# Kernel tuning notes

Hardware: AMD Instinct MI355X
Metric: run time of the kernel (lower is better)

Reference implementation:

```python
import math
import jax, jax.numpy as jnp
import numpy as np

DN = ('NCHW', 'OIHW', 'NCHW')

def _conv2d(x, w, b, stride, padding='VALID'):
    y = jax.lax.conv_general_dilated(x, w, window_strides=stride, padding=padding,
                                     dimension_numbers=DN)
    return y + b[None, :, None, None]

def _same_padding_conv(x, w, b, s):
    # replicate torch same_padding_conv: ceil-mode SAME padding, then VALID conv
    H, W = x.shape[2], x.shape[3]
    kh, kw = w.shape[2], w.shape[3]
    out_h, out_w = math.ceil(H / s[0]), math.ceil(W / s[1])
    pad_h = max((out_h - 1) * s[0] + kh - H, 0)
    pad_w = max((out_w - 1) * s[1] + kw - W, 0)
    pt, pl = pad_h // 2, pad_w // 2
    x = jnp.pad(x, ((0, 0), (0, 0), (pt, pad_h - pt), (pl, pad_w - pl)))
    return _conv2d(x, w, b, s)

def _leaky(x):
    return jax.nn.leaky_relu(x, negative_slope=0.2)

def setup_inputs() -> dict:
    key = jax.random.key(0)
    ks = jax.random.split(key, 8)
    B, cin, cout, H, W = 2, 16, 24, 384, 1280
    fl = jax.random.normal(ks[0], (B, cin, H, W), jnp.float32)
    fr = jax.random.normal(ks[1], (B, cin, H, W), jnp.float32)
    w_em = jax.random.normal(ks[2], (cout, cin, 4, 4), jnp.float32) * 0.05
    b_em = jax.random.normal(ks[3], (cout,), jnp.float32) * 0.05
    w_rc = jax.random.normal(ks[4], (cout, cout, 1, 1), jnp.float32) * 0.1
    b_rc = jax.random.normal(ks[5], (cout,), jnp.float32) * 0.05
    w_tf = jax.random.normal(ks[6], (13, cout + 1, 1, 1), jnp.float32) * 0.1
    b_tf = jax.random.normal(ks[7], (13,), jnp.float32) * 0.05
    return {'feature_left': fl, 'feature_right': fr, 'max_disp': 64,
            'w_em': w_em, 'b_em': b_em, 'w_rc': w_rc, 'b_rc': b_rc,
            'w_tf': w_tf, 'b_tf': b_tf}

def reference(feature_left, feature_right, max_disp, w_em, b_em, w_rc, b_rc, w_tf, b_tf):
    # left branch: 4x4 conv, stride (4,4), VALID (torch default padding=0)
    fl = _leaky(_conv2d(_leaky(_conv2d(feature_left, w_em, b_em, (4, 4))), w_rc, b_rc, (1, 1)))
    # right branch: same-padding conv with stride (4,1) -> full width retained
    fr = _leaky(_conv2d(_leaky(_same_padding_conv(feature_right, w_em, b_em, (4, 1))), w_rc, b_rc, (1, 1)))
    B, C, Hq, Wq = fl.shape
    Wr = fr.shape[3]
    # clipped gather indices: idx[d, x] = clip(4*x - d + 1, 0, Wr-1)
    d = jnp.arange(max_disp)[:, None]          # [D,1]
    x = jnp.arange(Wq)[None, :]                # [1,Wq]
    idx = jnp.clip(4 * x - d + 1, 0, Wr - 1)   # [D,Wq]
    fr_g = jnp.take(fr, idx, axis=3)           # [B,C,H,D,Wq]
    # L1 cost over channels -> [B,D,H,Wq]
    cost_volume = jnp.sum(jnp.abs(fl[:, :, :, None, :] - fr_g), axis=1).transpose(0, 2, 1, 3)
    cost_f = jnp.min(cost_volume, axis=1, keepdims=True)                  # [B,1,H,Wq]
    d_init = jnp.argmin(cost_volume, axis=1, keepdims=True).astype(fl.dtype)
    p_init = jnp.concatenate([cost_f, fl], axis=1)
    p_init = _leaky(_conv2d(p_init, w_tf, b_tf, (1, 1)))                  # [B,13,H,Wq]
    z = jnp.zeros_like(d_init)
    out = jnp.concatenate([d_init, z, z, p_init], axis=1)                 # [B,16,H,Wq]
    return out, cost_volume
```

## Files before the change

kernel.cpp:

```cpp
#include <hip/hip_runtime.h>

#define B_   2
#define CIN  16
#define HIN  384
#define WIN  1280
#define CO   24
#define HQ   96
#define WL   320
#define WR   1280
#define DMAX 64

__device__ __forceinline__ float lk(float v) { return v >= 0.f ? v : 0.2f * v; }

__global__ __launch_bounds__(256) void k_left(
    const float* __restrict__ x, const float* __restrict__ w_em,
    const float* __restrict__ b_em, const float* __restrict__ w_rc,
    const float* __restrict__ b_rc, float* __restrict__ out)
{
    __shared__ float smem[CO * CIN * 16];
    __shared__ __align__(16) float swt[CO * CO];
    __shared__ float sbe[CO], sbr[CO];

    for (int i = threadIdx.x; i < CO * CIN * 16; i += 256) smem[i] = w_em[i];
    for (int i = threadIdx.x; i < CO * CO; i += 256) swt[i] = w_rc[(i % CO) * CO + (i / CO)];
    if (threadIdx.x < CO) { sbe[threadIdx.x] = b_em[threadIdx.x]; sbr[threadIdx.x] = b_rc[threadIdx.x]; }
    __syncthreads();

    const int t = threadIdx.x;
    const int half = t >> 7, pxl = t & 127;
    const int obase = half * 12;
    const int flat = blockIdx.x * 128 + pxl;
    const int j = flat % WL, h = (flat / WL) % HQ, b = flat / (WL * HQ);

    float acc[12];
#pragma unroll
    for (int oo = 0; oo < 12; ++oo) acc[oo] = sbe[obase + oo];

    for (int c = 0; c < CIN; ++c) {
#pragma unroll
        for (int kh = 0; kh < 4; ++kh) {
            const float4 v = *(const float4*)(x + ((size_t)(b * CIN + c) * HIN + 4 * h + kh) * WIN + 4 * j);
#pragma unroll
            for (int oo = 0; oo < 12; ++oo) {
                const float4 wv = *(const float4*)&smem[(((obase + oo) * CIN + c) * 4 + kh) * 4];
                float a = acc[oo];
                a = fmaf(v.x, wv.x, a);
                a = fmaf(v.y, wv.y, a);
                a = fmaf(v.z, wv.z, a);
                a = fmaf(v.w, wv.w, a);
                acc[oo] = a;
            }
        }
    }
    __syncthreads();
#pragma unroll
    for (int oo = 0; oo < 12; ++oo) smem[(obase + oo) * 128 + pxl] = lk(acc[oo]);
    __syncthreads();

    float acc2[12];
#pragma unroll
    for (int oo = 0; oo < 12; ++oo) acc2[oo] = sbr[obase + oo];
    for (int c = 0; c < CO; ++c) {
        const float in_c = smem[c * 128 + pxl];
#pragma unroll
        for (int m = 0; m < 3; ++m) {
            const float4 wv = *(const float4*)&swt[c * CO + obase + 4 * m];
            acc2[4 * m + 0] = fmaf(in_c, wv.x, acc2[4 * m + 0]);
            acc2[4 * m + 1] = fmaf(in_c, wv.y, acc2[4 * m + 1]);
            acc2[4 * m + 2] = fmaf(in_c, wv.z, acc2[4 * m + 2]);
            acc2[4 * m + 3] = fmaf(in_c, wv.w, acc2[4 * m + 3]);
        }
    }
#pragma unroll
    for (int oo = 0; oo < 12; ++oo)
        out[((size_t)(b * CO + obase + oo) * HQ + h) * WL + j] = lk(acc2[oo]);
}

__global__ __launch_bounds__(256) void k_right(
    const float* __restrict__ x, const float* __restrict__ w_em,
    const float* __restrict__ b_em, const float* __restrict__ w_rc,
    const float* __restrict__ b_rc, float* __restrict__ out)
{
    __shared__ __align__(16) float sw[CO * CIN * 16];
    __shared__ __align__(16) float swt[CO * CO];
    __shared__ float sbe[CO], sbr[CO];

    for (int i = threadIdx.x; i < CO * CIN * 16; i += 256) sw[i] = w_em[i];
    for (int i = threadIdx.x; i < CO * CO; i += 256) swt[i] = w_rc[(i % CO) * CO + (i / CO)];
    if (threadIdx.x < CO) { sbe[threadIdx.x] = b_em[threadIdx.x]; sbr[threadIdx.x] = b_rc[threadIdx.x]; }
    __syncthreads();

    const int t = threadIdx.x;
    const int L = t & 63, quarter = t >> 6;
    const int obase = quarter * 6;
    const int row = blockIdx.x / 5, jbase = (blockIdx.x % 5) * 256;
    const int b = row / HQ, h = row % HQ;

    const bool vm1 = (jbase + 4 * L) > 0;
    const bool vp  = (jbase + 4 * L + 4) < WIN;
    const int  om1 = vm1 ? (4 * L - 2) : 0;
    const int  op4 = vp  ? (4 * L + 4) : 0;

    float acc[4][6];
#pragma unroll
    for (int k = 0; k < 4; ++k)
#pragma unroll
        for (int oo = 0; oo < 6; ++oo) acc[k][oo] = sbe[obase + oo];

    for (int c = 0; c < CIN; ++c) {
#pragma unroll
        for (int kh = 0; kh < 4; ++kh) {
            const float* xr = x + ((size_t)(b * CIN + c) * HIN + 4 * h + kh) * WIN + jbase;
            const float4  v = *(const float4*)(xr + 4 * L);
            const float2  A = *(const float2*)(xr + om1);
            const float2  C = *(const float2*)(xr + op4);
            float in[7];
            in[0] = vm1 ? A.y : 0.f;
            in[1] = v.x; in[2] = v.y; in[3] = v.z; in[4] = v.w;
            in[5] = vp ? C.x : 0.f;
            in[6] = vp ? C.y : 0.f;
#pragma unroll
            for (int oo = 0; oo < 6; ++oo) {
                const float4 wv = *(const float4*)&sw[(((obase + oo) * CIN + c) * 4 + kh) * 4];
#pragma unroll
                for (int k = 0; k < 4; ++k) {
                    float a = acc[k][oo];
                    a = fmaf(in[k],     wv.x, a);
                    a = fmaf(in[k + 1], wv.y, a);
                    a = fmaf(in[k + 2], wv.z, a);
                    a = fmaf(in[k + 3], wv.w, a);
                    acc[k][oo] = a;
                }
            }
        }
    }
    __syncthreads();
#pragma unroll
    for (int oo = 0; oo < 6; ++oo) {
        float4 st = make_float4(lk(acc[0][oo]), lk(acc[1][oo]), lk(acc[2][oo]), lk(acc[3][oo]));
        *(float4*)&sw[(obase + oo) * 256 + 4 * L] = st;
    }
    __syncthreads();

    float acc2[CO];
#pragma unroll
    for (int o = 0; o < CO; ++o) acc2[o] = sbr[o];
    for (int c = 0; c < CO; ++c) {
        const float in_c = sw[c * 256 + t];
#pragma unroll
        for (int m = 0; m < 6; ++m) {
            const float4 wv = *(const float4*)&swt[c * CO + 4 * m];
            acc2[4 * m + 0] = fmaf(in_c, wv.x, acc2[4 * m + 0]);
            acc2[4 * m + 1] = fmaf(in_c, wv.y, acc2[4 * m + 1]);
            acc2[4 * m + 2] = fmaf(in_c, wv.z, acc2[4 * m + 2]);
            acc2[4 * m + 3] = fmaf(in_c, wv.w, acc2[4 * m + 3]);
        }
    }
#pragma unroll
    for (int o = 0; o < CO; ++o)
        out[((size_t)(b * CO + o) * HQ + h) * WR + jbase + t] = lk(acc2[o]);
}

__global__ __launch_bounds__(256) void k_cost(
    const float* __restrict__ fl, const float* __restrict__ fr,
    const float* __restrict__ wtf, const float* __restrict__ btf,
    float* __restrict__ out, float* __restrict__ cost)
{
    __shared__ float frs[CO * 324];
    __shared__ float sbest[256];
    __shared__ int   sbd[256];

    const int t  = threadIdx.x;
    const int j  = t & 63;
    const int w  = t >> 6;
    const int jc = blockIdx.x % 5;
    const int r  = blockIdx.x / 5;
    const int h  = r % HQ, b = r / HQ;
    const int j0 = jc * 64;
    const int jg = j0 + j;
    const int colbase = 4 * j0 - 64;

    for (int idx = t; idx < CO * 320; idx += 256) {
        const int c = idx / 320, Wd = idx % 320;
        const int col = colbase + Wd;
        frs[c * 324 + 2 + Wd] = fr[((size_t)(b * CO + c) * HQ + h) * WR + (col > 0 ? col : 0)];
    }
    __syncthreads();

    float acc[4][4];
#pragma unroll
    for (int q = 0; q < 4; ++q)
#pragma unroll
        for (int rr = 0; rr < 4; ++rr) acc[q][rr] = 0.f;

    for (int c = 0; c < CO; ++c) {
        const float flc = fl[((size_t)(b * CO + c) * HQ + h) * WL + jg];
        const float* base = &frs[c * 324 + 4 * j + 64];
#pragma unroll
        for (int q = 0; q < 4; ++q) {
            const int D = 4 * w + q;
            const float4 v = *(const float4*)(base - 4 * D);
            acc[q][0] += fabsf(flc - v.w);
            acc[q][1] += fabsf(flc - v.z);
            acc[q][2] += fabsf(flc - v.y);
            acc[q][3] += fabsf(flc - v.x);
        }
    }

#pragma unroll
    for (int q = 0; q < 4; ++q)
#pragma unroll
        for (int rr = 0; rr < 4; ++rr) {
            const int d = 16 * w + 4 * q + rr;
            cost[((size_t)(b * DMAX + d) * HQ + h) * WL + jg] = acc[q][rr];
        }

    float best = acc[0][0]; int bd = 16 * w;
#pragma unroll
    for (int q = 0; q < 4; ++q)
#pragma unroll
        for (int rr = 0; rr < 4; ++rr) {
            if (q == 0 && rr == 0) continue;
            const int d = 16 * w + 4 * q + rr;
            if (acc[q][rr] < best) { best = acc[q][rr]; bd = d; }
        }
    sbest[t] = best; sbd[t] = bd;
    __syncthreads();

    if (t < 64) {
        float cur = sbest[j]; int curd = sbd[j];
#pragma unroll
        for (int g = 1; g < 4; ++g) {
            const float v = sbest[g * 64 + j];
            if (v < cur) { cur = v; curd = sbd[g * 64 + j]; }
        }
        float flr[CO];
#pragma unroll
        for (int c = 0; c < CO; ++c) flr[c] = fl[((size_t)(b * CO + c) * HQ + h) * WL + jg];
#pragma unroll
        for (int o = 0; o < 13; ++o) {
            float a = btf[o] + wtf[o * 25] * cur;
#pragma unroll
            for (int c = 0; c < CO; ++c) a += wtf[o * 25 + 1 + c] * flr[c];
            out[((size_t)(b * 16 + 3 + o) * HQ + h) * WL + jg] = lk(a);
        }
        out[((size_t)(b * 16 + 0) * HQ + h) * WL + jg] = (float)curd;
        out[((size_t)(b * 16 + 1) * HQ + h) * WL + jg] = 0.f;
        out[((size_t)(b * 16 + 2) * HQ + h) * WL + jg] = 0.f;
    }
}

extern "C" void kernel_launch(void* const* d_in, const int* in_sizes, int n_in,
                              void* d_out, int out_size, void* d_ws, size_t ws_size,
                              hipStream_t stream) {
    const float* fl_in = (const float*)d_in[0];
    const float* fr_in = (const float*)d_in[1];
    const float* w_em = (const float*)d_in[3];
    const float* b_em = (const float*)d_in[4];
    const float* w_rc = (const float*)d_in[5];
    const float* b_rc = (const float*)d_in[6];
    const float* w_tf = (const float*)d_in[7];
    const float* b_tf = (const float*)d_in[8];

    float* out  = (float*)d_out;
    float* cost = out + (size_t)B_ * 16 * HQ * WL;

    float* fl_ws = (float*)d_ws;
    float* fr_ws = fl_ws + (size_t)B_ * CO * HQ * WL;

    hipLaunchKernelGGL(k_right, dim3(960), dim3(256), 0, stream,
                       fr_in, w_em, b_em, w_rc, b_rc, fr_ws);
    hipLaunchKernelGGL(k_left,  dim3(480), dim3(256), 0, stream,
                       fl_in, w_em, b_em, w_rc, b_rc, fl_ws);
    hipLaunchKernelGGL(k_cost,  dim3(960), dim3(256), 0, stream,
                       fl_ws, fr_ws, w_tf, b_tf, out, cost);
}
```

Measured before the change: 252.1 us.

## Retile cost kernel for two-pixel register reuse and spread tail conv over warps

The cost-volume kernel now gives each thread two adjacent output columns and eight disparities. This lets it reuse overlapping right-feature float4 loads from shared memory and issue vectorized float2 loads and stores. The final 13-output 1x1 conv is split across all four wavefronts instead of one, which removes a serial tail. The left kernel's fma chains are also rewritten as plain multiply-add expressions, and the float4 weight reads in the second conv become scalar reads. The argmin now reduces over 8 groups, and changed float summation order in the left kernel may alter rounding slightly.

```diff
diff --git a/kernel.cpp b/kernel.cpp
--- a/kernel.cpp
+++ b/kernel.cpp
@@ -18,7 +18,7 @@
     const float* __restrict__ b_rc, float* __restrict__ out)
 {
     __shared__ float smem[CO * CIN * 16];
-    __shared__ __align__(16) float swt[CO * CO];
+    __shared__ float swt[CO * CO];
     __shared__ float sbe[CO], sbr[CO];
 
     for (int i = threadIdx.x; i < CO * CIN * 16; i += 256) smem[i] = w_em[i];
@@ -43,12 +43,7 @@
 #pragma unroll
             for (int oo = 0; oo < 12; ++oo) {
                 const float4 wv = *(const float4*)&smem[(((obase + oo) * CIN + c) * 4 + kh) * 4];
-                float a = acc[oo];
-                a = fmaf(v.x, wv.x, a);
-                a = fmaf(v.y, wv.y, a);
-                a = fmaf(v.z, wv.z, a);
-                a = fmaf(v.w, wv.w, a);
-                acc[oo] = a;
+                acc[oo] += v.x * wv.x + v.y * wv.y + v.z * wv.z + v.w * wv.w;
             }
         }
     }
@@ -63,13 +58,7 @@
     for (int c = 0; c < CO; ++c) {
         const float in_c = smem[c * 128 + pxl];
 #pragma unroll
-        for (int m = 0; m < 3; ++m) {
-            const float4 wv = *(const float4*)&swt[c * CO + obase + 4 * m];
-            acc2[4 * m + 0] = fmaf(in_c, wv.x, acc2[4 * m + 0]);
-            acc2[4 * m + 1] = fmaf(in_c, wv.y, acc2[4 * m + 1]);
-            acc2[4 * m + 2] = fmaf(in_c, wv.z, acc2[4 * m + 2]);
-            acc2[4 * m + 3] = fmaf(in_c, wv.w, acc2[4 * m + 3]);
-        }
+        for (int oo = 0; oo < 12; ++oo) acc2[oo] += in_c * swt[c * CO + obase + oo];
     }
 #pragma unroll
     for (int oo = 0; oo < 12; ++oo)
@@ -167,18 +156,18 @@
     float* __restrict__ out, float* __restrict__ cost)
 {
     __shared__ float frs[CO * 324];
-    __shared__ float sbest[256];
-    __shared__ int   sbd[256];
+    __shared__ float sbest[8 * 64];
+    __shared__ int   sbd[8 * 64];
 
     const int t  = threadIdx.x;
-    const int j  = t & 63;
-    const int w  = t >> 6;
+    const int p  = t & 31;
+    const int g  = t >> 5;
     const int jc = blockIdx.x % 5;
     const int r  = blockIdx.x / 5;
     const int h  = r % HQ, b = r / HQ;
     const int j0 = jc * 64;
-    const int jg = j0 + j;
     const int colbase = 4 * j0 - 64;
+    const int cA = 2 * p;
 
     for (int idx = t; idx < CO * 320; idx += 256) {
         const int c = idx / 320, Wd = idx % 320;
@@ -187,63 +176,73 @@
     }
     __syncthreads();
 
-    float acc[4][4];
-#pragma unroll
-    for (int q = 0; q < 4; ++q)
-#pragma unroll
-        for (int rr = 0; rr < 4; ++rr) acc[q][rr] = 0.f;
+    float accA[8], accB[8];
+#pragma unroll
+    for (int dd = 0; dd < 8; ++dd) { accA[dd] = 0.f; accB[dd] = 0.f; }
 
     for (int c = 0; c < CO; ++c) {
-        const float flc = fl[((size_t)(b * CO + c) * HQ + h) * WL + jg];
-        const float* base = &frs[c * 324 + 4 * j + 64];
-#pragma unroll
-        for (int q = 0; q < 4; ++q) {
-            const int D = 4 * w + q;
-            const float4 v = *(const float4*)(base - 4 * D);
-            acc[q][0] += fabsf(flc - v.w);
-            acc[q][1] += fabsf(flc - v.z);
-            acc[q][2] += fabsf(flc - v.y);
-            acc[q][3] += fabsf(flc - v.x);
-        }
-    }
-
-#pragma unroll
-    for (int q = 0; q < 4; ++q)
-#pragma unroll
-        for (int rr = 0; rr < 4; ++rr) {
-            const int d = 16 * w + 4 * q + rr;
-            cost[((size_t)(b * DMAX + d) * HQ + h) * WL + jg] = acc[q][rr];
-        }
-
-    float best = acc[0][0]; int bd = 16 * w;
-#pragma unroll
-    for (int q = 0; q < 4; ++q)
-#pragma unroll
-        for (int rr = 0; rr < 4; ++rr) {
-            if (q == 0 && rr == 0) continue;
-            const int d = 16 * w + 4 * q + rr;
-            if (acc[q][rr] < best) { best = acc[q][rr]; bd = d; }
-        }
-    sbest[t] = best; sbd[t] = bd;
-    __syncthreads();
-
-    if (t < 64) {
-        float cur = sbest[j]; int curd = sbd[j];
-#pragma unroll
-        for (int g = 1; g < 4; ++g) {
-            const float v = sbest[g * 64 + j];
-            if (v < cur) { cur = v; curd = sbd[g * 64 + j]; }
-        }
-        float flr[CO];
-#pragma unroll
-        for (int c = 0; c < CO; ++c) flr[c] = fl[((size_t)(b * CO + c) * HQ + h) * WL + jg];
-#pragma unroll
-        for (int o = 0; o < 13; ++o) {
-            float a = btf[o] + wtf[o * 25] * cur;
-#pragma unroll
-            for (int c = 0; c < CO; ++c) a += wtf[o * 25 + 1 + c] * flr[c];
-            out[((size_t)(b * 16 + 3 + o) * HQ + h) * WL + jg] = lk(a);
-        }
+        const float2 flc = *(const float2*)&fl[((size_t)(b * CO + c) * HQ + h) * WL + j0 + cA];
+        const float* base = &frs[c * 324 + 8 * p - 8 * g + 60];
+        const float4 F0 = *(const float4*)(base);
+        const float4 F1 = *(const float4*)(base + 4);
+        const float4 F2 = *(const float4*)(base + 8);
+        accA[0] += fabsf(flc.x - F1.w);
+        accA[1] += fabsf(flc.x - F1.z);
+        accA[2] += fabsf(flc.x - F1.y);
+        accA[3] += fabsf(flc.x - F1.x);
+        accA[4] += fabsf(flc.x - F0.w);
+        accA[5] += fabsf(flc.x - F0.z);
+        accA[6] += fabsf(flc.x - F0.y);
+        accA[7] += fabsf(flc.x - F0.x);
+        accB[0] += fabsf(flc.y - F2.w);
+        accB[1] += fabsf(flc.y - F2.z);
+        accB[2] += fabsf(flc.y - F2.y);
+        accB[3] += fabsf(flc.y - F2.x);
+        accB[4] += fabsf(flc.y - F1.w);
+        accB[5] += fabsf(flc.y - F1.z);
+        accB[6] += fabsf(flc.y - F1.y);
+        accB[7] += fabsf(flc.y - F1.x);
+    }
+
+#pragma unroll
+    for (int dd = 0; dd < 8; ++dd) {
+        const int d = 8 * g + dd;
+        float2 st = make_float2(accA[dd], accB[dd]);
+        *(float2*)&cost[((size_t)(b * DMAX + d) * HQ + h) * WL + j0 + cA] = st;
+    }
+
+    float bA = accA[0]; int dA = 8 * g;
+    float bB = accB[0]; int dB = 8 * g;
+#pragma unroll
+    for (int dd = 1; dd < 8; ++dd) {
+        if (accA[dd] < bA) { bA = accA[dd]; dA = 8 * g + dd; }
+        if (accB[dd] < bB) { bB = accB[dd]; dB = 8 * g + dd; }
+    }
+    sbest[g * 64 + cA]     = bA; sbd[g * 64 + cA]     = dA;
+    sbest[g * 64 + cA + 1] = bB; sbd[g * 64 + cA + 1] = dB;
+    __syncthreads();
+
+    const int j = t & 63, w = t >> 6;
+    const int jg = j0 + j;
+    float cur = sbest[j]; int curd = sbd[j];
+#pragma unroll
+    for (int g2 = 1; g2 < 8; ++g2) {
+        const float v = sbest[g2 * 64 + j];
+        if (v < cur) { cur = v; curd = sbd[g2 * 64 + j]; }
+    }
+    float flr[CO];
+#pragma unroll
+    for (int c = 0; c < CO; ++c) flr[c] = fl[((size_t)(b * CO + c) * HQ + h) * WL + jg];
+
+    const int o_lo = (w == 0) ? 0 : 4 * w - 3;
+    const int o_hi = 4 * w + 1;
+    for (int o = o_lo; o < o_hi; ++o) {
+        float a = btf[o] + wtf[o * 25] * cur;
+#pragma unroll
+        for (int c = 0; c < CO; ++c) a += wtf[o * 25 + 1 + c] * flr[c];
+        out[((size_t)(b * 16 + 3 + o) * HQ + h) * WL + jg] = lk(a);
+    }
+    if (w == 0) {
         out[((size_t)(b * 16 + 0) * HQ + h) * WL + jg] = (float)curd;
         out[((size_t)(b * 16 + 1) * HQ + h) * WL + jg] = 0.f;
         out[((size_t)(b * 16 + 2) * HQ + h) * WL + jg] = 0.f;
```

New measurement: 237.7 us. 5.7% less time.

## Merge left and right embedding kernels into one interleaved launch; spread 1x1 head across warps

Applied to the files above, without the earlier changes.

The separate left and right embedding kernels become one kernel of 1440 blocks. Every third block does a left tile and the rest do right tiles, so both branches run at once and one launch is removed. In the cost kernel, the final 13-output 1x1 conv is now split across all four wavefronts instead of only the first 64 threads. This cuts the serial tail, though every wavefront now reloads the 24 fl channels. The left path also swaps explicit fmaf chains for plain expressions, and mixing two block types in one kernel may raise register pressure.

```diff
diff --git a/kernel.cpp b/kernel.cpp
--- a/kernel.cpp
+++ b/kernel.cpp
@@ -12,153 +12,132 @@
 
 __device__ __forceinline__ float lk(float v) { return v >= 0.f ? v : 0.2f * v; }
 
-__global__ __launch_bounds__(256) void k_left(
-    const float* __restrict__ x, const float* __restrict__ w_em,
-    const float* __restrict__ b_em, const float* __restrict__ w_rc,
-    const float* __restrict__ b_rc, float* __restrict__ out)
+__global__ __launch_bounds__(256) void k_em(
+    const float* __restrict__ xl, const float* __restrict__ xr,
+    const float* __restrict__ w_em, const float* __restrict__ b_em,
+    const float* __restrict__ w_rc, const float* __restrict__ b_rc,
+    float* __restrict__ out_l, float* __restrict__ out_r)
 {
-    __shared__ float smem[CO * CIN * 16];
+    __shared__ __align__(16) float buf[CO * CIN * 16];
     __shared__ __align__(16) float swt[CO * CO];
     __shared__ float sbe[CO], sbr[CO];
 
-    for (int i = threadIdx.x; i < CO * CIN * 16; i += 256) smem[i] = w_em[i];
+    for (int i = threadIdx.x; i < CO * CIN * 16; i += 256) buf[i] = w_em[i];
     for (int i = threadIdx.x; i < CO * CO; i += 256) swt[i] = w_rc[(i % CO) * CO + (i / CO)];
     if (threadIdx.x < CO) { sbe[threadIdx.x] = b_em[threadIdx.x]; sbr[threadIdx.x] = b_rc[threadIdx.x]; }
     __syncthreads();
 
     const int t = threadIdx.x;
-    const int half = t >> 7, pxl = t & 127;
-    const int obase = half * 12;
-    const int flat = blockIdx.x * 128 + pxl;
-    const int j = flat % WL, h = (flat / WL) % HQ, b = flat / (WL * HQ);
-
-    float acc[12];
-#pragma unroll
-    for (int oo = 0; oo < 12; ++oo) acc[oo] = sbe[obase + oo];
-
-    for (int c = 0; c < CIN; ++c) {
-#pragma unroll
-        for (int kh = 0; kh < 4; ++kh) {
-            const float4 v = *(const float4*)(x + ((size_t)(b * CIN + c) * HIN + 4 * h + kh) * WIN + 4 * j);
-#pragma unroll
-            for (int oo = 0; oo < 12; ++oo) {
-                const float4 wv = *(const float4*)&smem[(((obase + oo) * CIN + c) * 4 + kh) * 4];
-                float a = acc[oo];
-                a = fmaf(v.x, wv.x, a);
-                a = fmaf(v.y, wv.y, a);
-                a = fmaf(v.z, wv.z, a);
-                a = fmaf(v.w, wv.w, a);
-                acc[oo] = a;
-            }
-        }
-    }
-    __syncthreads();
-#pragma unroll
-    for (int oo = 0; oo < 12; ++oo) smem[(obase + oo) * 128 + pxl] = lk(acc[oo]);
-    __syncthreads();
-
-    float acc2[12];
-#pragma unroll
-    for (int oo = 0; oo < 12; ++oo) acc2[oo] = sbr[obase + oo];
-    for (int c = 0; c < CO; ++c) {
-        const float in_c = smem[c * 128 + pxl];
-#pragma unroll
-        for (int m = 0; m < 3; ++m) {
-            const float4 wv = *(const float4*)&swt[c * CO + obase + 4 * m];
-            acc2[4 * m + 0] = fmaf(in_c, wv.x, acc2[4 * m + 0]);
-            acc2[4 * m + 1] = fmaf(in_c, wv.y, acc2[4 * m + 1]);
-            acc2[4 * m + 2] = fmaf(in_c, wv.z, acc2[4 * m + 2]);
-            acc2[4 * m + 3] = fmaf(in_c, wv.w, acc2[4 * m + 3]);
-        }
-    }
-#pragma unroll
-    for (int oo = 0; oo < 12; ++oo)
-        out[((size_t)(b * CO + obase + oo) * HQ + h) * WL + j] = lk(acc2[oo]);
-}
-
-__global__ __launch_bounds__(256) void k_right(
-    const float* __restrict__ x, const float* __restrict__ w_em,
-    const float* __restrict__ b_em, const float* __restrict__ w_rc,
-    const float* __restrict__ b_rc, float* __restrict__ out)
-{
-    __shared__ __align__(16) float sw[CO * CIN * 16];
-    __shared__ __align__(16) float swt[CO * CO];
-    __shared__ float sbe[CO], sbr[CO];
-
-    for (int i = threadIdx.x; i < CO * CIN * 16; i += 256) sw[i] = w_em[i];
-    for (int i = threadIdx.x; i < CO * CO; i += 256) swt[i] = w_rc[(i % CO) * CO + (i / CO)];
-    if (threadIdx.x < CO) { sbe[threadIdx.x] = b_em[threadIdx.x]; sbr[threadIdx.x] = b_rc[threadIdx.x]; }
-    __syncthreads();
-
-    const int t = threadIdx.x;
-    const int L = t & 63, quarter = t >> 6;
-    const int obase = quarter * 6;
-    const int row = blockIdx.x / 5, jbase = (blockIdx.x % 5) * 256;
-    const int b = row / HQ, h = row % HQ;
-
-    const bool vm1 = (jbase + 4 * L) > 0;
-    const bool vp  = (jbase + 4 * L + 4) < WIN;
-    const int  om1 = vm1 ? (4 * L - 2) : 0;
-    const int  op4 = vp  ? (4 * L + 4) : 0;
-
-    float acc[4][6];
-#pragma unroll
-    for (int k = 0; k < 4; ++k)
-#pragma unroll
-        for (int oo = 0; oo < 6; ++oo) acc[k][oo] = sbe[obase + oo];
-
-    for (int c = 0; c < CIN; ++c) {
-#pragma unroll
-        for (int kh = 0; kh < 4; ++kh) {
-            const float* xr = x + ((size_t)(b * CIN + c) * HIN + 4 * h + kh) * WIN + jbase;
-            const float4  v = *(const float4*)(xr + 4 * L);
-            const float2  A = *(const float2*)(xr + om1);
-            const float2  C = *(const float2*)(xr + op4);
-            float in[7];
-            in[0] = vm1 ? A.y : 0.f;
-            in[1] = v.x; in[2] = v.y; in[3] = v.z; in[4] = v.w;
-            in[5] = vp ? C.x : 0.f;
-            in[6] = vp ? C.y : 0.f;
-#pragma unroll
-            for (int oo = 0; oo < 6; ++oo) {
-                const float4 wv = *(const float4*)&sw[(((obase + oo) * CIN + c) * 4 + kh) * 4];
-#pragma unroll
-                for (int k = 0; k < 4; ++k) {
-                    float a = acc[k][oo];
-                    a = fmaf(in[k],     wv.x, a);
-                    a = fmaf(in[k + 1], wv.y, a);
-                    a = fmaf(in[k + 2], wv.z, a);
-                    a = fmaf(in[k + 3], wv.w, a);
-                    acc[k][oo] = a;
+
+    if (blockIdx.x % 3 == 0) {
+        const int lb = blockIdx.x / 3;
+        const int half = t >> 7, pxl = t & 127;
+        const int obase = half * 12;
+        const int flat = lb * 128 + pxl;
+        const int j = flat % WL, h = (flat / WL) % HQ, b = flat / (WL * HQ);
+
+        float acc[12];
+#pragma unroll
+        for (int oo = 0; oo < 12; ++oo) acc[oo] = sbe[obase + oo];
+
+        for (int c = 0; c < CIN; ++c) {
+#pragma unroll
+            for (int kh = 0; kh < 4; ++kh) {
+                const float4 v = *(const float4*)(xl + ((size_t)(b * CIN + c) * HIN + 4 * h + kh) * WIN + 4 * j);
+#pragma unroll
+                for (int oo = 0; oo < 12; ++oo) {
+                    const float4 wv = *(const float4*)&buf[(((obase + oo) * CIN + c) * 4 + kh) * 4];
+                    acc[oo] += v.x * wv.x + v.y * wv.y + v.z * wv.z + v.w * wv.w;
                 }
             }
         }
-    }
-    __syncthreads();
-#pragma unroll
-    for (int oo = 0; oo < 6; ++oo) {
-        float4 st = make_float4(lk(acc[0][oo]), lk(acc[1][oo]), lk(acc[2][oo]), lk(acc[3][oo]));
-        *(float4*)&sw[(obase + oo) * 256 + 4 * L] = st;
-    }
-    __syncthreads();
-
-    float acc2[CO];
-#pragma unroll
-    for (int o = 0; o < CO; ++o) acc2[o] = sbr[o];
-    for (int c = 0; c < CO; ++c) {
-        const float in_c = sw[c * 256 + t];
-#pragma unroll
-        for (int m = 0; m < 6; ++m) {
-            const float4 wv = *(const float4*)&swt[c * CO + 4 * m];
-            acc2[4 * m + 0] = fmaf(in_c, wv.x, acc2[4 * m + 0]);
-            acc2[4 * m + 1] = fmaf(in_c, wv.y, acc2[4 * m + 1]);
-            acc2[4 * m + 2] = fmaf(in_c, wv.z, acc2[4 * m + 2]);
-            acc2[4 * m + 3] = fmaf(in_c, wv.w, acc2[4 * m + 3]);
-        }
-    }
-#pragma unroll
-    for (int o = 0; o < CO; ++o)
-        out[((size_t)(b * CO + o) * HQ + h) * WR + jbase + t] = lk(acc2[o]);
+        __syncthreads();
+#pragma unroll
+        for (int oo = 0; oo < 12; ++oo) buf[(obase + oo) * 128 + pxl] = lk(acc[oo]);
+        __syncthreads();
+
+        float acc2[12];
+#pragma unroll
+        for (int oo = 0; oo < 12; ++oo) acc2[oo] = sbr[obase + oo];
+        for (int c = 0; c < CO; ++c) {
+            const float in_c = buf[c * 128 + pxl];
+#pragma unroll
+            for (int oo = 0; oo < 12; ++oo) acc2[oo] += in_c * swt[c * CO + obase + oo];
+        }
+#pragma unroll
+        for (int oo = 0; oo < 12; ++oo)
+            out_l[((size_t)(b * CO + obase + oo) * HQ + h) * WL + j] = lk(acc2[oo]);
+    } else {
+        const int rb = blockIdx.x - blockIdx.x / 3 - 1;
+        const int L = t & 63, quarter = t >> 6;
+        const int obase = quarter * 6;
+        const int row = rb / 5, jbase = (rb % 5) * 256;
+        const int b = row / HQ, h = row % HQ;
+
+        const bool vm1 = (jbase + 4 * L) > 0;
+        const bool vp  = (jbase + 4 * L + 4) < WIN;
+        const int  om1 = vm1 ? (4 * L - 2) : 0;
+        const int  op4 = vp  ? (4 * L + 4) : 0;
+
+        float acc[4][6];
+#pragma unroll
+        for (int k = 0; k < 4; ++k)
+#pragma unroll
+            for (int oo = 0; oo < 6; ++oo) acc[k][oo] = sbe[obase + oo];
+
+        for (int c = 0; c < CIN; ++c) {
+#pragma unroll
+            for (int kh = 0; kh < 4; ++kh) {
+                const float* xp = xr + ((size_t)(b * CIN + c) * HIN + 4 * h + kh) * WIN + jbase;
+                const float4  v = *(const float4*)(xp + 4 * L);
+                const float2  A = *(const float2*)(xp + om1);
+                const float2  C = *(const float2*)(xp + op4);
+                float in[7];
+                in[0] = vm1 ? A.y : 0.f;
+                in[1] = v.x; in[2] = v.y; in[3] = v.z; in[4] = v.w;
+                in[5] = vp ? C.x : 0.f;
+                in[6] = vp ? C.y : 0.f;
+#pragma unroll
+                for (int oo = 0; oo < 6; ++oo) {
+                    const float4 wv = *(const float4*)&buf[(((obase + oo) * CIN + c) * 4 + kh) * 4];
+#pragma unroll
+                    for (int k = 0; k < 4; ++k) {
+                        float a = acc[k][oo];
+                        a = fmaf(in[k],     wv.x, a);
+                        a = fmaf(in[k + 1], wv.y, a);
+                        a = fmaf(in[k + 2], wv.z, a);
+                        a = fmaf(in[k + 3], wv.w, a);
+                        acc[k][oo] = a;
+                    }
+                }
+            }
+        }
+        __syncthreads();
+#pragma unroll
+        for (int oo = 0; oo < 6; ++oo) {
+            float4 st = make_float4(lk(acc[0][oo]), lk(acc[1][oo]), lk(acc[2][oo]), lk(acc[3][oo]));
+            *(float4*)&buf[(obase + oo) * 256 + 4 * L] = st;
+        }
+        __syncthreads();
+
+        float acc2[CO];
+#pragma unroll
+        for (int o = 0; o < CO; ++o) acc2[o] = sbr[o];
+        for (int c = 0; c < CO; ++c) {
+            const float in_c = buf[c * 256 + t];
+#pragma unroll
+            for (int m = 0; m < 6; ++m) {
+                const float4 wv = *(const float4*)&swt[c * CO + 4 * m];
+                acc2[4 * m + 0] = fmaf(in_c, wv.x, acc2[4 * m + 0]);
+                acc2[4 * m + 1] = fmaf(in_c, wv.y, acc2[4 * m + 1]);
+                acc2[4 * m + 2] = fmaf(in_c, wv.z, acc2[4 * m + 2]);
+                acc2[4 * m + 3] = fmaf(in_c, wv.w, acc2[4 * m + 3]);
+            }
+        }
+#pragma unroll
+        for (int o = 0; o < CO; ++o)
+            out_r[((size_t)(b * CO + o) * HQ + h) * WR + jbase + t] = lk(acc2[o]);
+    }
 }
 
 __global__ __launch_bounds__(256) void k_cost(
@@ -227,23 +206,25 @@
     sbest[t] = best; sbd[t] = bd;
     __syncthreads();
 
-    if (t < 64) {
-        float cur = sbest[j]; int curd = sbd[j];
-#pragma unroll
-        for (int g = 1; g < 4; ++g) {
-            const float v = sbest[g * 64 + j];
-            if (v < cur) { cur = v; curd = sbd[g * 64 + j]; }
-        }
-        float flr[CO];
-#pragma unroll
-        for (int c = 0; c < CO; ++c) flr[c] = fl[((size_t)(b * CO + c) * HQ + h) * WL + jg];
-#pragma unroll
-        for (int o = 0; o < 13; ++o) {
-            float a = btf[o] + wtf[o * 25] * cur;
-#pragma unroll
-            for (int c = 0; c < CO; ++c) a += wtf[o * 25 + 1 + c] * flr[c];
-            out[((size_t)(b * 16 + 3 + o) * HQ + h) * WL + jg] = lk(a);
-        }
+    float cur = sbest[j]; int curd = sbd[j];
+#pragma unroll
+    for (int g = 1; g < 4; ++g) {
+        const float v = sbest[g * 64 + j];
+        if (v < cur) { cur = v; curd = sbd[g * 64 + j]; }
+    }
+    float flr[CO];
+#pragma unroll
+    for (int c = 0; c < CO; ++c) flr[c] = fl[((size_t)(b * CO + c) * HQ + h) * WL + jg];
+
+    const int o_lo = (w == 0) ? 0 : 4 * w - 3;
+    const int o_hi = 4 * w + 1;
+    for (int o = o_lo; o < o_hi; ++o) {
+        float a = btf[o] + wtf[o * 25] * cur;
+#pragma unroll
+        for (int c = 0; c < CO; ++c) a += wtf[o * 25 + 1 + c] * flr[c];
+        out[((size_t)(b * 16 + 3 + o) * HQ + h) * WL + jg] = lk(a);
+    }
+    if (w == 0) {
         out[((size_t)(b * 16 + 0) * HQ + h) * WL + jg] = (float)curd;
         out[((size_t)(b * 16 + 1) * HQ + h) * WL + jg] = 0.f;
         out[((size_t)(b * 16 + 2) * HQ + h) * WL + jg] = 0.f;
@@ -268,10 +249,8 @@
     float* fl_ws = (float*)d_ws;
     float* fr_ws = fl_ws + (size_t)B_ * CO * HQ * WL;
 
-    hipLaunchKernelGGL(k_right, dim3(960), dim3(256), 0, stream,
-                       fr_in, w_em, b_em, w_rc, b_rc, fr_ws);
-    hipLaunchKernelGGL(k_left,  dim3(480), dim3(256), 0, stream,
-                       fl_in, w_em, b_em, w_rc, b_rc, fl_ws);
-    hipLaunchKernelGGL(k_cost,  dim3(960), dim3(256), 0, stream,
+    hipLaunchKernelGGL(k_em, dim3(1440), dim3(256), 0, stream,
+                       fl_in, fr_in, w_em, b_em, w_rc, b_rc, fl_ws, fr_ws);
+    hipLaunchKernelGGL(k_cost, dim3(960), dim3(256), 0, stream,
                        fl_ws, fr_ws, w_tf, b_tf, out, cost);
 }
```

New measurement: 237.1 us. 1.06x faster.
